# Optimization experiments

Hardware: AMD Instinct MI355X
Metric: run time of the kernel (lower is better)

## Reference

```python
import jax, jax.numpy as jnp
import numpy as np


def setup_inputs() -> dict:
    key = jax.random.key(0)
    k1, k2, k3 = jax.random.split(key, 3)
    B, L, C, D, V = 8, 512, 4000, 512, 10000
    x = jax.random.uniform(k1, (B, L, C), dtype=jnp.float32)            # dense char n-gram features
    W_proj = jax.random.normal(k2, (D, C), dtype=jnp.float32) * 0.02     # Linear(char_vsize, d_vec), no bias
    emb_matrix = jax.random.uniform(k3, (V, D), dtype=jnp.float32,
                                    minval=-0.1, maxval=0.1)             # QueryEmb latent embedding table
    return {"x": x, "W_proj": W_proj, "emb_matrix": emb_matrix}


def reference(x, W_proj, emb_matrix):
    # charEmbedder: tanh(Linear(x)) per sentence -> vectorized over batch
    q = jnp.tanh(jnp.einsum('blc,dc->bld', x, W_proj))                   # [B, L, D]
    # QueryEmb: softmax(q @ E^T) @ E + q  (dropout in eval mode = identity)
    attn = jax.nn.softmax(jnp.einsum('bld,vd->blv', q, emb_matrix), axis=-1)  # [B, L, V]
    ctx = jnp.einsum('blv,vd->bld', attn, emb_matrix) + q                # residual
    return ctx
```

## Files before the change

kernel.cpp:

```cpp
#include <hip/hip_runtime.h>
#include <hip/hip_bf16.h>

typedef unsigned short u16;
typedef unsigned int u32;
typedef unsigned char u8;
typedef __bf16 bf16x8 __attribute__((ext_vector_type(8)));
typedef u16 u16x8 __attribute__((ext_vector_type(8)));
typedef float f32x4 __attribute__((ext_vector_type(4)));
typedef u32 u32x4 __attribute__((ext_vector_type(4)));
typedef u32 u32x2 __attribute__((ext_vector_type(2)));
typedef long longx2 __attribute__((ext_vector_type(2)));

#define MM   4096
#define CC   4000
#define KP   4096
#define DD   512
#define VV   10000
#define VPAD 10240

#define WS8_QB   0u
#define WS8_QF   4194304u
#define WS8_EF   6291456u
#define WS8_ETF  11534336u
#define WS8_LACC 16777216u
#define WS8_R    16793600u
#define R_XB     0u
#define R_WB     33554432u
#define R_QA     37748736u
#define WS8_PACC 88096768u
#define FAST8_NEED 155205632u

#define WS_Q    0u
#define WS_EB   4194304u
#define WS_ET   14680064u
#define WS_LACC 25165824u
#define WS_P    25182208u

__device__ __forceinline__ u16 f2bf(float f) {
  u32 u = __builtin_bit_cast(u32, f);
  return (u16)((u + 0x7FFFu + ((u >> 16) & 1u)) >> 16);
}
__device__ __forceinline__ float bf2f(u16 h) {
  u32 u = (u32)h << 16;
  return __builtin_bit_cast(float, u);
}
__device__ __forceinline__ u8 f2fp8(float f) {
  u32 u = __builtin_bit_cast(u32, f);
  u32 s = (u >> 31) << 7;
  u32 m = u & 0x7FFFFFFFu;
  if (m < 0x3C800000u) return (u8)s;
  u32 r = m + 0x7FFFFu + ((m >> 20) & 1u);
  return (u8)(((r >> 20) - 960u) | s);
}
__device__ __forceinline__ u32 pk4fp8(float f0, float f1, float f2, float f3) {
#if __has_builtin(__builtin_amdgcn_cvt_pk_fp8_f32)
  int w = 0;
  w = __builtin_amdgcn_cvt_pk_fp8_f32(f0, f1, w, false);
  w = __builtin_amdgcn_cvt_pk_fp8_f32(f2, f3, w, true);
  return (u32)w;
#else
  return (u32)f2fp8(f0) | ((u32)f2fp8(f1) << 8) |
         ((u32)f2fp8(f2) << 16) | ((u32)f2fp8(f3) << 24);
#endif
}

#define GLDS(gp, lp) __builtin_amdgcn_global_load_lds( \
    (const __attribute__((address_space(1))) void*)(gp), \
    (__attribute__((address_space(3))) void*)(lp), 16, 0, 0)

__device__ __forceinline__ int fr16(int row, int q) {
  return row * 64 + (((q ^ ((row >> 1) & 3)) << 4));
}
__device__ __forceinline__ int pgrp(int j) { return (j & 3) * 2 + (j >> 2); }


__global__ __launch_bounds__(256) void k_eprep8(const float* __restrict__ E,
                                                u8* __restrict__ Ef,
                                                u8* __restrict__ ETf,
                                                float* __restrict__ Lacc) {
  __shared__ u8 st[64 * 68];
  int tid = threadIdx.x;
  {
    int flat = blockIdx.x * 8 + blockIdx.y;
    int fid = flat * 256 + tid;
    if (fid < MM) Lacc[fid] = 0.f;
  }
  int v0 = blockIdx.x * 64, d0 = blockIdx.y * 64;
  int r = tid >> 2, seg = tid & 3;
  u32 w[4];
  int v = v0 + r;
  if (v < VV) {
    const float* src = E + (size_t)v * DD + d0 + seg * 16;
    #pragma unroll
    for (int j = 0; j < 4; ++j) {
      float4 t = *(const float4*)(src + j * 4);
      w[j] = pk4fp8(t.x * 16.f, t.y * 16.f, t.z * 16.f, t.w * 16.f);
    }
  } else {
    #pragma unroll
    for (int j = 0; j < 4; ++j) w[j] = 0;
  }
  int g0 = pgrp(2 * seg), g1 = pgrp(2 * seg + 1);
  {
    size_t rowb = (size_t)v * DD + d0;
    u32x2 a = {w[0], w[1]}, b = {w[2], w[3]};
    *(u32x2*)(Ef + rowb + g0 * 8) = a;
    *(u32x2*)(Ef + rowb + g1 * 8) = b;
  }
  #pragma unroll
  for (int j = 0; j < 4; ++j)
    *(u32*)&st[r * 68 + seg * 16 + j * 4] = w[j];
  __syncthreads();
  {
    u8 g[16];
    #pragma unroll
    for (int j = 0; j < 16; ++j) g[j] = st[(seg * 16 + j) * 68 + r];
    u32 t[4];
    #pragma unroll
    for (int q = 0; q < 4; ++q)
      t[q] = (u32)g[4*q] | ((u32)g[4*q+1] << 8) | ((u32)g[4*q+2] << 16) | ((u32)g[4*q+3] << 24);
    size_t rowb = (size_t)(d0 + r) * VPAD + v0;
    u32x2 a = {t[0], t[1]}, b = {t[2], t[3]};
    *(u32x2*)(ETf + rowb + g0 * 8) = a;
    *(u32x2*)(ETf + rowb + g1 * 8) = b;
  }
}

__global__ __launch_bounds__(256) void k_conv(const float* __restrict__ X,
                                              const float* __restrict__ Wp,
                                              u16* __restrict__ Xb,
                                              u16* __restrict__ Wb) {
  int row = blockIdx.x;
  int t = threadIdx.x;
  const float* src;
  u16* dst;
  if (row < MM) { src = X + (size_t)row * CC; dst = Xb + (size_t)row * KP; }
  else { src = Wp + (size_t)(row - MM) * CC; dst = Wb + (size_t)(row - MM) * KP; }
  int c0 = t * 16;
  u16 h[16];
  if (c0 + 16 <= CC) {
    #pragma unroll
    for (int j = 0; j < 4; ++j) {
      float4 v = *(const float4*)(src + c0 + j * 4);
      h[4*j+0] = f2bf(v.x); h[4*j+1] = f2bf(v.y); h[4*j+2] = f2bf(v.z); h[4*j+3] = f2bf(v.w);
    }
  } else {
    #pragma unroll
    for (int j = 0; j < 16; ++j) h[j] = 0;
  }
  u16x8 p0, p1;
  #pragma unroll
  for (int j = 0; j < 8; ++j) { p0[j] = h[j]; p1[j] = h[8+j]; }
  *(u16x8*)(dst + c0) = p0; *(u16x8*)(dst + c0 + 8) = p1;
}

__global__ __launch_bounds__(256) void k_g1(const u16* __restrict__ Xb,
                                            const u16* __restrict__ Wb,
                                            float* __restrict__ Qacc) {
  __shared__ u16 As[128 * 64];
  __shared__ u16 Bs[64 * 64];
  int tid = threadIdx.x;
  int m0 = blockIdx.x * 128;
  int n0 = blockIdx.y * 64;
  int kt0 = blockIdx.z * 16;
  int w = tid >> 6, l = tid & 63;
  int l15 = l & 15, quad = l >> 4;
  int lr = l >> 3, lg = l & 7;
  f32x4 acc[2][4] = {};

  for (int kt = kt0; kt < kt0 + 16; ++kt) {
    #pragma unroll
    for (int i = 0; i < 4; ++i) {
      int wc = i * 4 + w;
      int row = wc * 8 + lr;
      int g = lg ^ (row & 7);
      GLDS(Xb + (size_t)(m0 + row) * KP + kt * 64 + g * 8, As + wc * 512);
      if (i < 2)
        GLDS(Wb + (size_t)(n0 + row) * KP + kt * 64 + g * 8, Bs + wc * 512);
    }
    __syncthreads();
    #pragma unroll
    for (int kk = 0; kk < 2; ++kk) {
      bf16x8 a[2], b[4];
      #pragma unroll
      for (int mi = 0; mi < 2; ++mi) {
        int arow = w * 32 + mi * 16 + l15;
        int slot = (kk * 4 + quad) ^ (arow & 7);
        a[mi] = *(const bf16x8*)&As[arow * 64 + slot * 8];
      }
      #pragma unroll
      for (int ni = 0; ni < 4; ++ni) {
        int brow = ni * 16 + l15;
        int slot = (kk * 4 + quad) ^ (brow & 7);
        b[ni] = *(const bf16x8*)&Bs[brow * 64 + slot * 8];
      }
      #pragma unroll
      for (int mi = 0; mi < 2; ++mi)
        #pragma unroll
        for (int ni = 0; ni < 4; ++ni)
          acc[mi][ni] = __builtin_amdgcn_mfma_f32_16x16x32_bf16(a[mi], b[ni], acc[mi][ni], 0, 0, 0);
    }
    __syncthreads();
  }
  float* dst = Qacc + (size_t)blockIdx.z * (MM * DD);
  #pragma unroll
  for (int mi = 0; mi < 2; ++mi)
    #pragma unroll
    for (int ni = 0; ni < 4; ++ni)
      #pragma unroll
      for (int r = 0; r < 4; ++r) {
        int m = m0 + w * 32 + mi * 16 + quad * 4 + r;
        int d = n0 + ni * 16 + l15;
        dst[(size_t)m * DD + d] = acc[mi][ni][r];
      }
}

__global__ __launch_bounds__(256) void k_tanh4(const float* __restrict__ Qacc,
                                               u16* __restrict__ Qb,
                                               u8* __restrict__ Qf) {
  int idx = blockIdx.x * 256 + threadIdx.x;
  size_t base = (size_t)idx * 8;
  f32x4 s0 = {0,0,0,0}, s1 = {0,0,0,0};
  #pragma unroll
  for (int z = 0; z < 4; ++z) {
    s0 += *(const f32x4*)(Qacc + (size_t)z * (MM * DD) + base);
    s1 += *(const f32x4*)(Qacc + (size_t)z * (MM * DD) + base + 4);
  }
  float t[8];
  #pragma unroll
  for (int j = 0; j < 4; ++j) t[j] = tanhf(s0[j]);
  #pragma unroll
  for (int j = 0; j < 4; ++j) t[4+j] = tanhf(s1[j]);
  u16x8 p;
  #pragma unroll
  for (int j = 0; j < 8; ++j) p[j] = f2bf(t[j]);
  *(u16x8*)(Qb + base) = p;
  u32x2 q8;
  q8[0] = pk4fp8(t[0] * 4.f, t[1] * 4.f, t[2] * 4.f, t[3] * 4.f);
  q8[1] = pk4fp8(t[4] * 4.f, t[5] * 4.f, t[6] * 4.f, t[7] * 4.f);
  int jg = (int)((base >> 3) & 7);
  size_t dest = (base & ~(size_t)63) + (size_t)pgrp(jg) * 8;
  *(u32x2*)(Qf + dest) = q8;
}

__global__ __launch_bounds__(256, 4) void k_s8(const u8* __restrict__ Qf,
                                               const u8* __restrict__ Ef,
                                               u8* __restrict__ Pf,
                                               float* __restrict__ Lacc) {
  __shared__ u8 S8[16384];
  u8* As = S8;
  u8* Bs = S8 + 8192;
  int tid = threadIdx.x;
  int m0 = blockIdx.x * 128;
  int n0 = blockIdx.y * 128;
  int w = tid >> 6, l = tid & 63;
  int l15 = l & 15, quad = l >> 4;
  int mhalf = w >> 1, nhalf = w & 1;
  int srow = tid >> 2, schunk = tid & 3;
  int sw = schunk ^ ((srow >> 1) & 3);
  const u8* qa0 = Qf + (size_t)(m0 + srow) * DD + sw * 16;
  const u8* qa1 = Qf + (size_t)(m0 + 64 + srow) * DD + sw * 16;
  const u8* eb0 = Ef + (size_t)(n0 + srow) * DD + sw * 16;
  const u8* eb1 = Ef + (size_t)(n0 + 64 + srow) * DD + sw * 16;
  f32x4 acc[4][4] = {};

  for (int kt = 0; kt < 8; ++kt) {
    GLDS(qa0 + kt * 64, As + tid * 16);
    GLDS(qa1 + kt * 64, As + 4096 + tid * 16);
    GLDS(eb0 + kt * 64, Bs + tid * 16);
    GLDS(eb1 + kt * 64, Bs + 4096 + tid * 16);
    __syncthreads();
    longx2 a[4], b[4];
    #pragma unroll
    for (int mi = 0; mi < 4; ++mi)
      a[mi] = *(const longx2*)&As[fr16(mhalf * 64 + mi * 16 + l15, quad)];
    #pragma unroll
    for (int ni = 0; ni < 4; ++ni)
      b[ni] = *(const longx2*)&Bs[fr16(nhalf * 64 + ni * 16 + l15, quad)];
    #pragma unroll
    for (int mi = 0; mi < 4; ++mi)
      #pragma unroll
      for (int ni = 0; ni < 4; ++ni)
        acc[mi][ni] = __builtin_amdgcn_mfma_f32_16x16x32_fp8_fp8(a[mi][0], b[ni][0], acc[mi][ni], 0, 0, 0);
    #pragma unroll
    for (int mi = 0; mi < 4; ++mi)
      #pragma unroll
      for (int ni = 0; ni < 4; ++ni)
        acc[mi][ni] = __builtin_amdgcn_mfma_f32_16x16x32_fp8_fp8(a[mi][1], b[ni][1], acc[mi][ni], 0, 0, 0);
    __syncthreads();
  }

  const float C2 = 0.0225421100138901f;
  float rs[4][4] = {};
  #pragma unroll
  for (int mi = 0; mi < 4; ++mi) {
    #pragma unroll
    for (int ni = 0; ni < 4; ++ni) {
      bool ok = (n0 + nhalf * 64 + ni * 16 + l15) < VV;
      int p_in = ((ni & 1) * 2 + (l15 >> 3)) * 16 + ((ni >> 1) << 3) + (l15 & 7);
      int gbyte = nhalf * 64 + p_in;
      int gch = gbyte >> 4, glo = gbyte & 15;
      float pf[4];
      #pragma unroll
      for (int r = 0; r < 4; ++r) {
        float t = fminf(fmaf(acc[mi][ni][r], C2, -2.f), 6.3f);
        float p = ok ? exp2f(t) : 0.f;
        pf[r] = p;
        rs[mi][r] += p;
      }
      u32 wpk = pk4fp8(pf[0], pf[1], pf[2], pf[3]);
      #pragma unroll
      for (int r = 0; r < 4; ++r) {
        int rowL = mhalf * 64 + mi * 16 + quad * 4 + r;
        S8[rowL * 128 + ((gch ^ (rowL & 7)) << 4) + glo] = (u8)(wpk >> (8 * r));
      }
    }
  }
  __syncthreads();
  {
    int row = tid >> 1, h2 = tid & 1;
    size_t gbase = (size_t)(m0 + row) * VPAD + n0 + h2 * 64;
    #pragma unroll
    for (int c = 0; c < 4; ++c) {
      int slot = h2 * 4 + c;
      *(u32x4*)(Pf + gbase + c * 16) =
          *(const u32x4*)&S8[row * 128 + ((slot ^ (row & 7)) << 4)];
    }
  }
  #pragma unroll
  for (int mi = 0; mi < 4; ++mi)
    #pragma unroll
    for (int r = 0; r < 4; ++r) {
      float v = rs[mi][r];
      v += __shfl_xor(v, 1, 16);
      v += __shfl_xor(v, 2, 16);
      v += __shfl_xor(v, 4, 16);
      v += __shfl_xor(v, 8, 16);
      if (l15 == 0)
        atomicAdd(&Lacc[m0 + mhalf * 64 + mi * 16 + quad * 4 + r], v);
    }
}

__global__ __launch_bounds__(256, 4) void k_pvs8(const u8* __restrict__ Pf,
                                                 const u8* __restrict__ ETf,
                                                 float* __restrict__ Pacc) {
  __shared__ u8 S8[16384];
  u8* As = S8;
  u8* Bs = S8 + 8192;
  int tid = threadIdx.x;
  int m0 = blockIdx.x * 128;
  int d0 = blockIdx.y * 128;
  int z = blockIdx.z;
  int w = tid >> 6, l = tid & 63;
  int l15 = l & 15, quad = l >> 4;
  int mhalf = w >> 1, nhalf = w & 1;
  int srow = tid >> 2, schunk = tid & 3;
  int sw = schunk ^ ((srow >> 1) & 3);
  const u8* pa0 = Pf + (size_t)(m0 + srow) * VPAD + sw * 16;
  const u8* pa1 = Pf + (size_t)(m0 + 64 + srow) * VPAD + sw * 16;
  const u8* eb0 = ETf + (size_t)(d0 + srow) * VPAD + sw * 16;
  const u8* eb1 = ETf + (size_t)(d0 + 64 + srow) * VPAD + sw * 16;
  f32x4 acc[4][4] = {};
  int kt0 = z * 20;

  for (int kt = kt0; kt < kt0 + 20; ++kt) {
    GLDS(pa0 + kt * 64, As + tid * 16);
    GLDS(pa1 + kt * 64, As + 4096 + tid * 16);
    GLDS(eb0 + kt * 64, Bs + tid * 16);
    GLDS(eb1 + kt * 64, Bs + 4096 + tid * 16);
    __syncthreads();
    longx2 a[4], b[4];
    #pragma unroll
    for (int mi = 0; mi < 4; ++mi)
      a[mi] = *(const longx2*)&As[fr16(mhalf * 64 + mi * 16 + l15, quad)];
    #pragma unroll
    for (int ni = 0; ni < 4; ++ni)
      b[ni] = *(const longx2*)&Bs[fr16(nhalf * 64 + ni * 16 + l15, quad)];
    #pragma unroll
    for (int mi = 0; mi < 4; ++mi)
      #pragma unroll
      for (int ni = 0; ni < 4; ++ni)
        acc[mi][ni] = __builtin_amdgcn_mfma_f32_16x16x32_fp8_fp8(a[mi][0], b[ni][0], acc[mi][ni], 0, 0, 0);
    #pragma unroll
    for (int mi = 0; mi < 4; ++mi)
      #pragma unroll
      for (int ni = 0; ni < 4; ++ni)
        acc[mi][ni] = __builtin_amdgcn_mfma_f32_16x16x32_fp8_fp8(a[mi][1], b[ni][1], acc[mi][ni], 0, 0, 0);
    __syncthreads();
  }
  float* dst = Pacc + (size_t)z * (MM * DD);
  #pragma unroll
  for (int mi = 0; mi < 4; ++mi)
    #pragma unroll
    for (int ni = 0; ni < 4; ++ni)
      #pragma unroll
      for (int r = 0; r < 4; ++r) {
        int m = m0 + mhalf * 64 + mi * 16 + quad * 4 + r;
        int d = d0 + nhalf * 64 + ni * 16 + l15;
        dst[(size_t)m * DD + d] = acc[mi][ni][r];
      }
}

__global__ __launch_bounds__(256) void k_fin8v2(float* __restrict__ Out,
                                                const float* __restrict__ Lacc,
                                                const u16* __restrict__ Qb,
                                                const float* __restrict__ Pacc) {
  int idx = blockIdx.x * 256 + threadIdx.x;
  int m = idx >> 7;
  int d4 = (idx & 127) * 4;
  float inv = 0.0625f / Lacc[m];
  size_t off = (size_t)m * DD + d4;
  f32x4 s = {0.f, 0.f, 0.f, 0.f};
  #pragma unroll
  for (int z = 0; z < 8; ++z)
    s += *(const f32x4*)(Pacc + (size_t)z * (MM * DD) + off);
  const u16* qp = Qb + off;
  f32x4 r;
  #pragma unroll
  for (int i = 0; i < 4; ++i) r[i] = s[i] * inv + bf2f(qp[i]);
  *(f32x4*)(Out + off) = r;
}


__global__ __launch_bounds__(256) void k_eprep(const float* __restrict__ E,
                                               u16* __restrict__ Eb,
                                               u16* __restrict__ ETb,
                                               float* __restrict__ Out,
                                               float* __restrict__ Lacc) {
  __shared__ u16 st[64 * 65];
  int tid = threadIdx.x;
  {
    int bid = blockIdx.x * 8 + blockIdx.y;
    f32x4 z = {0.f, 0.f, 0.f, 0.f};
    #pragma unroll
    for (int rep = 0; rep < 2; ++rep) {
      int id = bid * 256 + tid + rep * 327680;
      if (id < 524288)      *(f32x4*)(Out + (size_t)id * 4) = z;
      else if (id < 525312) *(f32x4*)(Lacc + (size_t)(id - 524288) * 4) = z;
    }
  }
  int v0 = blockIdx.x * 64, d0 = blockIdx.y * 64;
  int r = tid >> 2, seg = tid & 3;
  u16 h[16];
  int v = v0 + r;
  if (v < VV) {
    const float* src = E + (size_t)v * DD + d0 + seg * 16;
    #pragma unroll
    for (int j = 0; j < 4; ++j) {
      float4 t = *(const float4*)(src + j * 4);
      h[4*j+0] = f2bf(t.x); h[4*j+1] = f2bf(t.y); h[4*j+2] = f2bf(t.z); h[4*j+3] = f2bf(t.w);
    }
  } else {
    #pragma unroll
    for (int j = 0; j < 16; ++j) h[j] = 0;
  }
  {
    u16x8 p0, p1;
    #pragma unroll
    for (int j = 0; j < 8; ++j) { p0[j] = h[j]; p1[j] = h[8+j]; }
    u16* dst = Eb + (size_t)v * DD + d0 + seg * 16;
    *(u16x8*)dst = p0; *(u16x8*)(dst + 8) = p1;
  }
  #pragma unroll
  for (int j = 0; j < 16; ++j) st[r * 65 + seg * 16 + j] = h[j];
  __syncthreads();
  {
    u16 g[16];
    #pragma unroll
    for (int j = 0; j < 16; ++j) g[j] = st[(seg * 16 + j) * 65 + r];
    u16x8 p0, p1;
    #pragma unroll
    for (int j = 0; j < 8; ++j) { p0[j] = g[j]; p1[j] = g[8+j]; }
    u16* dst = ETb + (size_t)(d0 + r) * VPAD + v0 + seg * 16;
    *(u16x8*)dst = p0; *(u16x8*)(dst + 8) = p1;
  }
}

__global__ __launch_bounds__(256) void k_gemm1(const float* __restrict__ X,
                                               const float* __restrict__ W,
                                               u16* __restrict__ Qb) {
  __shared__ u16 xs[64 * 64];
  __shared__ u16 wst[64 * 64];
  int tid = threadIdx.x;
  int m0 = blockIdx.x * 64;
  int n0 = blockIdx.y * 64;
  int srow = tid >> 2;
  int sseg = tid & 3;
  int r7 = srow & 7;
  const float* xsrc = X + (size_t)(m0 + srow) * CC + sseg * 16;
  const float* wsrc = W + (size_t)(n0 + srow) * CC + sseg * 16;
  int lane = tid & 63;
  int wv = tid >> 6;
  int l15 = lane & 15, quad = lane >> 4;
  f32x4 acc[4] = {};

  for (int kt = 0; kt < 63; ++kt) {
    int cbase = kt * 64 + sseg * 16;
    float xv[16], wf[16];
    if (cbase + 16 <= CC) {
      #pragma unroll
      for (int j = 0; j < 4; ++j) {
        float4 tx = *(const float4*)(xsrc + kt * 64 + j * 4);
        float4 tw = *(const float4*)(wsrc + kt * 64 + j * 4);
        xv[4*j+0] = tx.x; xv[4*j+1] = tx.y; xv[4*j+2] = tx.z; xv[4*j+3] = tx.w;
        wf[4*j+0] = tw.x; wf[4*j+1] = tw.y; wf[4*j+2] = tw.z; wf[4*j+3] = tw.w;
      }
    } else {
      #pragma unroll
      for (int j = 0; j < 16; ++j) { xv[j] = 0.f; wf[j] = 0.f; }
    }
    __syncthreads();
    #pragma unroll
    for (int j = 0; j < 2; ++j) {
      int g = (sseg * 2 + j) ^ r7;
      u16x8 px, pw;
      #pragma unroll
      for (int e = 0; e < 8; ++e) { px[e] = f2bf(xv[8*j+e]); pw[e] = f2bf(wf[8*j+e]); }
      *(u16x8*)&xs[srow * 64 + (g << 3)] = px;
      *(u16x8*)&wst[srow * 64 + (g << 3)] = pw;
    }
    __syncthreads();
    #pragma unroll
    for (int kk = 0; kk < 2; ++kk) {
      int arow = 16 * wv + l15;
      int ga = (kk * 4 + quad) ^ (arow & 7);
      bf16x8 a = *(const bf16x8*)&xs[arow * 64 + (ga << 3)];
      #pragma unroll
      for (int nb = 0; nb < 4; ++nb) {
        int brow = 16 * nb + l15;
        int gb = (kk * 4 + quad) ^ (brow & 7);
        bf16x8 b = *(const bf16x8*)&wst[brow * 64 + (gb << 3)];
        acc[nb] = __builtin_amdgcn_mfma_f32_16x16x32_bf16(a, b, acc[nb], 0, 0, 0);
      }
    }
  }
  #pragma unroll
  for (int nb = 0; nb < 4; ++nb) {
    int d = n0 + 16 * nb + l15;
    #pragma unroll
    for (int r = 0; r < 4; ++r) {
      int m = m0 + 16 * wv + 4 * quad + r;
      Qb[(size_t)m * DD + d] = f2bf(tanhf(acc[nb][r]));
    }
  }
}

__global__ __launch_bounds__(256) void k_s(const u16* __restrict__ Qb,
                                           const u16* __restrict__ Eb,
                                           u16* __restrict__ Pg,
                                           float* __restrict__ Lacc,
                                           int cbase, int W) {
  __shared__ u16 As[128 * 64];
  __shared__ u16 Bs[128 * 64];
  int tid = threadIdx.x;
  int m0 = blockIdx.x * 128;
  int n0 = blockIdx.y * 128;
  int w = tid >> 6, l = tid & 63;
  int l15 = l & 15, quad = l >> 4;
  int mhalf = w >> 1, nhalf = w & 1;
  int lr = l >> 3, lg = l & 7;
  f32x4 acc[4][4] = {};

  for (int kt = 0; kt < 8; ++kt) {
    #pragma unroll
    for (int i = 0; i < 4; ++i) {
      int wc = i * 4 + w;
      int row = wc * 8 + lr;
      int g = lg ^ (row & 7);
      GLDS(Qb + (size_t)(m0 + row) * DD + kt * 64 + g * 8, As + wc * 512);
      GLDS(Eb + (size_t)(cbase + n0 + row) * DD + kt * 64 + g * 8, Bs + wc * 512);
    }
    __syncthreads();
    #pragma unroll
    for (int kk = 0; kk < 2; ++kk) {
      bf16x8 a[4], b[4];
      #pragma unroll
      for (int mi = 0; mi < 4; ++mi) {
        int arow = mhalf * 64 + mi * 16 + l15;
        int slot = (kk * 4 + quad) ^ (arow & 7);
        a[mi] = *(const bf16x8*)&As[arow * 64 + slot * 8];
      }
      #pragma unroll
      for (int ni = 0; ni < 4; ++ni) {
        int brow = nhalf * 64 + ni * 16 + l15;
        int slot = (kk * 4 + quad) ^ (brow & 7);
        b[ni] = *(const bf16x8*)&Bs[brow * 64 + slot * 8];
      }
      #pragma unroll
      for (int mi = 0; mi < 4; ++mi)
        #pragma unroll
        for (int ni = 0; ni < 4; ++ni)
          acc[mi][ni] = __builtin_amdgcn_mfma_f32_16x16x32_bf16(a[mi], b[ni], acc[mi][ni], 0, 0, 0);
    }
    __syncthreads();
  }

  float rs[4][4] = {};
  #pragma unroll
  for (int mi = 0; mi < 4; ++mi) {
    #pragma unroll
    for (int ni = 0; ni < 4; ++ni) {
      int ncol = n0 + nhalf * 64 + ni * 16 + l15;
      bool ok = (cbase + ncol) < VV;
      #pragma unroll
      for (int r = 0; r < 4; ++r) {
        float p = ok ? __expf(acc[mi][ni][r]) : 0.f;
        rs[mi][r] += p;
        int m = m0 + mhalf * 64 + mi * 16 + quad * 4 + r;
        Pg[(size_t)m * W + ncol] = f2bf(p);
      }
    }
  }
  #pragma unroll
  for (int mi = 0; mi < 4; ++mi)
    #pragma unroll
    for (int r = 0; r < 4; ++r) {
      float v = rs[mi][r];
      v += __shfl_xor(v, 1, 16);
      v += __shfl_xor(v, 2, 16);
      v += __shfl_xor(v, 4, 16);
      v += __shfl_xor(v, 8, 16);
      if (l15 == 0)
        atomicAdd(&Lacc[m0 + mhalf * 64 + mi * 16 + quad * 4 + r], v);
    }
}

__global__ __launch_bounds__(256) void k_pv(const u16* __restrict__ Pg,
                                            const u16* __restrict__ ETb,
                                            float* __restrict__ Out,
                                            int cbase, int W) {
  __shared__ u16 As[128 * 64];
  __shared__ u16 Bs[64 * 64];
  int tid = threadIdx.x;
  int m0 = blockIdx.x * 128;
  int n0 = blockIdx.y * 64;
  int w = tid >> 6, l = tid & 63;
  int l15 = l & 15, quad = l >> 4;
  int lr = l >> 3, lg = l & 7;
  int iters = W >> 6;
  f32x4 acc[2][4] = {};

  for (int kt = 0; kt < iters; ++kt) {
    #pragma unroll
    for (int i = 0; i < 4; ++i) {
      int wc = i * 4 + w;
      int row = wc * 8 + lr;
      int g = lg ^ (row & 7);
      GLDS(Pg + (size_t)(m0 + row) * W + kt * 64 + g * 8, As + wc * 512);
      if (i < 2)
        GLDS(ETb + (size_t)(n0 + row) * VPAD + cbase + kt * 64 + g * 8, Bs + wc * 512);
    }
    __syncthreads();
    #pragma unroll
    for (int kk = 0; kk < 2; ++kk) {
      bf16x8 a[2], b[4];
      #pragma unroll
      for (int mi = 0; mi < 2; ++mi) {
        int arow = w * 32 + mi * 16 + l15;
        int slot = (kk * 4 + quad) ^ (arow & 7);
        a[mi] = *(const bf16x8*)&As[arow * 64 + slot * 8];
      }
      #pragma unroll
      for (int ni = 0; ni < 4; ++ni) {
        int brow = ni * 16 + l15;
        int slot = (kk * 4 + quad) ^ (brow & 7);
        b[ni] = *(const bf16x8*)&Bs[brow * 64 + slot * 8];
      }
      #pragma unroll
      for (int mi = 0; mi < 2; ++mi)
        #pragma unroll
        for (int ni = 0; ni < 4; ++ni)
          acc[mi][ni] = __builtin_amdgcn_mfma_f32_16x16x32_bf16(a[mi], b[ni], acc[mi][ni], 0, 0, 0);
    }
    __syncthreads();
  }
  #pragma unroll
  for (int mi = 0; mi < 2; ++mi)
    #pragma unroll
    for (int ni = 0; ni < 4; ++ni)
      #pragma unroll
      for (int r = 0; r < 4; ++r) {
        int m = m0 + w * 32 + mi * 16 + quad * 4 + r;
        int d = n0 + ni * 16 + l15;
        Out[(size_t)m * DD + d] += acc[mi][ni][r];
      }
}

__global__ __launch_bounds__(256) void k_fin(float* __restrict__ Out,
                                             const float* __restrict__ Lacc,
                                             const u16* __restrict__ Qb) {
  int idx = blockIdx.x * 256 + threadIdx.x;
  int m = idx >> 7;
  int d4 = (idx & 127) * 4;
  float inv = 1.f / Lacc[m];
  f32x4 ov = *(const f32x4*)(Out + (size_t)m * DD + d4);
  const u16* qp = Qb + (size_t)m * DD + d4;
  f32x4 r;
  #pragma unroll
  for (int i = 0; i < 4; ++i) r[i] = ov[i] * inv + bf2f(qp[i]);
  *(f32x4*)(Out + (size_t)m * DD + d4) = r;
}

extern "C" void kernel_launch(void* const* d_in, const int* in_sizes, int n_in,
                              void* d_out, int out_size, void* d_ws, size_t ws_size,
                              hipStream_t stream) {
  const float* x  = (const float*)d_in[0];
  const float* Wp = (const float*)d_in[1];
  const float* E  = (const float*)d_in[2];
  float* out = (float*)d_out;
  char* ws = (char*)d_ws;

  if (ws_size >= (size_t)FAST8_NEED) {
    u16*   Qb   = (u16*)(ws + WS8_QB);
    u8*    Qf   = (u8*)(ws + WS8_QF);
    u8*    Ef   = (u8*)(ws + WS8_EF);
    u8*    ETf  = (u8*)(ws + WS8_ETF);
    float* Lacc = (float*)(ws + WS8_LACC);
    u16*   Xb   = (u16*)(ws + WS8_R + R_XB);
    u16*   Wb   = (u16*)(ws + WS8_R + R_WB);
    float* Qacc = (float*)(ws + WS8_R + R_QA);
    u8*    Pf   = (u8*)(ws + WS8_R);
    float* Pacc = (float*)(ws + WS8_PACC);

    k_eprep8<<<dim3(VPAD / 64, DD / 64), 256, 0, stream>>>(E, Ef, ETf, Lacc);
    k_conv<<<dim3(MM + DD), 256, 0, stream>>>(x, Wp, Xb, Wb);
    k_g1<<<dim3(MM / 128, DD / 64, 4), 256, 0, stream>>>(Xb, Wb, Qacc);
    k_tanh4<<<dim3(MM * DD / 8 / 256), 256, 0, stream>>>(Qacc, Qb, Qf);
    k_s8<<<dim3(MM / 128, VPAD / 128), 256, 0, stream>>>(Qf, Ef, Pf, Lacc);
    k_pvs8<<<dim3(MM / 128, DD / 128, 8), 256, 0, stream>>>(Pf, ETf, Pacc);
    k_fin8v2<<<dim3(MM * DD / 4 / 256), 256, 0, stream>>>(out, Lacc, Qb, Pacc);
  } else {
    u16*   Qb   = (u16*)(ws + WS_Q);
    u16*   Eb   = (u16*)(ws + WS_EB);
    u16*   ETb  = (u16*)(ws + WS_ET);
    float* Lacc = (float*)(ws + WS_LACC);
    u16*   Pc   = (u16*)(ws + WS_P);
    int W = 640;
    if (ws_size >= (size_t)WS_P + (size_t)MM * 2560 * 2) W = 2560;
    else if (ws_size >= (size_t)WS_P + (size_t)MM * 1280 * 2) W = 1280;
    int nch = VPAD / W;
    k_eprep<<<dim3(VPAD / 64, DD / 64), 256, 0, stream>>>(E, Eb, ETb, out, Lacc);
    k_gemm1<<<dim3(MM / 64, DD / 64), 256, 0, stream>>>(x, Wp, Qb);
    for (int c = 0; c < nch; ++c) {
      k_s <<<dim3(MM / 128, W / 128), 256, 0, stream>>>(Qb, Eb, Pc, Lacc, c * W, W);
      k_pv<<<dim3(MM / 128, DD / 64), 256, 0, stream>>>(Pc, ETb, out, c * W, W);
    }
    k_fin<<<dim3(MM * DD / 4 / 256), 256, 0, stream>>>(out, Lacc, Qb);
  }
}
```

Before: 256.9 us.

## Write FP8 probability tiles directly to global memory without LDS staging

The exponent epilogue now packs four column values per row into one 32-bit word and stores it straight to the global P buffer. This removes the LDS scatter, the barrier and the 16-byte readback. The transposed embedding pre-pass also changes its gather order so each thread writes one 16-byte vector instead of two 8-byte chunks. Both writers change the byte permutation of the stored FP8 data, so the consuming MFMA kernel's layout assumptions must still match. The direct global stores are narrower, 4 bytes each, and less coalesced.

```diff
diff --git a/kernel.cpp b/kernel.cpp
--- a/kernel.cpp
+++ b/kernel.cpp
@@ -100,8 +100,8 @@
     #pragma unroll
     for (int j = 0; j < 4; ++j) w[j] = 0;
   }
-  int g0 = pgrp(2 * seg), g1 = pgrp(2 * seg + 1);
   {
+    int g0 = pgrp(2 * seg), g1 = pgrp(2 * seg + 1);
     size_t rowb = (size_t)v * DD + d0;
     u32x2 a = {w[0], w[1]}, b = {w[2], w[3]};
     *(u32x2*)(Ef + rowb + g0 * 8) = a;
@@ -114,15 +114,15 @@
   {
     u8 g[16];
     #pragma unroll
-    for (int j = 0; j < 16; ++j) g[j] = st[(seg * 16 + j) * 68 + r];
-    u32 t[4];
+    for (int u = 0; u < 16; ++u) {
+      int c = 16 * (u & 3) + 4 * seg + (u >> 2);
+      g[u] = st[c * 68 + r];
+    }
+    u32x4 p;
     #pragma unroll
     for (int q = 0; q < 4; ++q)
-      t[q] = (u32)g[4*q] | ((u32)g[4*q+1] << 8) | ((u32)g[4*q+2] << 16) | ((u32)g[4*q+3] << 24);
-    size_t rowb = (size_t)(d0 + r) * VPAD + v0;
-    u32x2 a = {t[0], t[1]}, b = {t[2], t[3]};
-    *(u32x2*)(ETf + rowb + g0 * 8) = a;
-    *(u32x2*)(ETf + rowb + g1 * 8) = b;
+      p[q] = (u32)g[4*q] | ((u32)g[4*q+1] << 8) | ((u32)g[4*q+2] << 16) | ((u32)g[4*q+3] << 24);
+    *(u32x4*)(ETf + (size_t)(d0 + r) * VPAD + v0 + seg * 16) = p;
   }
 }
 
@@ -292,39 +292,22 @@
 
   const float C2 = 0.0225421100138901f;
   float rs[4][4] = {};
+  int boff = n0 + nhalf * 64 + (l15 >> 2) * 16 + (l15 & 3) * 4;
   #pragma unroll
   for (int mi = 0; mi < 4; ++mi) {
     #pragma unroll
-    for (int ni = 0; ni < 4; ++ni) {
-      bool ok = (n0 + nhalf * 64 + ni * 16 + l15) < VV;
-      int p_in = ((ni & 1) * 2 + (l15 >> 3)) * 16 + ((ni >> 1) << 3) + (l15 & 7);
-      int gbyte = nhalf * 64 + p_in;
-      int gch = gbyte >> 4, glo = gbyte & 15;
+    for (int r = 0; r < 4; ++r) {
+      int m = m0 + mhalf * 64 + mi * 16 + quad * 4 + r;
       float pf[4];
       #pragma unroll
-      for (int r = 0; r < 4; ++r) {
+      for (int ni = 0; ni < 4; ++ni) {
+        bool ok = (n0 + nhalf * 64 + ni * 16 + l15) < VV;
         float t = fminf(fmaf(acc[mi][ni][r], C2, -2.f), 6.3f);
         float p = ok ? exp2f(t) : 0.f;
-        pf[r] = p;
+        pf[ni] = p;
         rs[mi][r] += p;
       }
-      u32 wpk = pk4fp8(pf[0], pf[1], pf[2], pf[3]);
-      #pragma unroll
-      for (int r = 0; r < 4; ++r) {
-        int rowL = mhalf * 64 + mi * 16 + quad * 4 + r;
-        S8[rowL * 128 + ((gch ^ (rowL & 7)) << 4) + glo] = (u8)(wpk >> (8 * r));
-      }
-    }
-  }
-  __syncthreads();
-  {
-    int row = tid >> 1, h2 = tid & 1;
-    size_t gbase = (size_t)(m0 + row) * VPAD + n0 + h2 * 64;
-    #pragma unroll
-    for (int c = 0; c < 4; ++c) {
-      int slot = h2 * 4 + c;
-      *(u32x4*)(Pf + gbase + c * 16) =
-          *(const u32x4*)&S8[row * 128 + ((slot ^ (row & 7)) << 4)];
+      *(u32*)(Pf + (size_t)m * VPAD + boff) = pk4fp8(pf[0], pf[1], pf[2], pf[3]);
     }
   }
   #pragma unroll
```

Measured after the change: 257.6 us. No clear change (+0.2%).
